# Optimization experiments

Measured on AMD Instinct MI355X. Metric: run time of the kernel, lower is better.

Reference implementation:

```python
import jax, jax.numpy as jnp
import numpy as np

EPS = 1e-5

def _layernorm(x, g, b):
    # normalize over last (channel) axis
    mu = jnp.mean(x, axis=-1, keepdims=True)
    var = jnp.var(x, axis=-1, keepdims=True)
    return (x - mu) * jax.lax.rsqrt(var + EPS) * g + b

def _dynamix(xt, wnd, bnd, wnn, bnn):
    # xt: [B, M, N, C]; mixes over the N axis (vectorized form of the per-slice loop)
    B, M, N, C = xt.shape
    d = wnd.shape[1]
    p = xt @ wnd + bnd                       # [B,M,N,d]
    p = p.reshape(B, M, N * d) @ wnn + bnn   # [B,M,N*N]
    p = jax.nn.softmax(p.reshape(B, M, N, N), axis=-1)
    return jnp.einsum('bmij,bmjc->bmic', p, xt)  # [B,M,N,C]

def setup_inputs() -> dict:
    key = jax.random.key(0)
    ks = jax.random.split(key, 10)
    B, C, H, W, d, E = 32, 128, 56, 56, 10, 4
    def n(k, shape, scale=0.02):
        return jax.random.normal(k, shape, jnp.float32) * scale
    return {
        'x': jax.random.normal(ks[0], (B, C, H, W), jnp.float32),
        'ln1_g': jnp.ones((C,), jnp.float32), 'ln1_b': jnp.zeros((C,), jnp.float32),
        'h_wnd': n(ks[1], (C, d)), 'h_bnd': jnp.zeros((d,), jnp.float32),
        'h_wnn': n(ks[2], (W * d, W * W)), 'h_bnn': jnp.zeros((W * W,), jnp.float32),
        'w_wnd': n(ks[3], (C, d)), 'w_bnd': jnp.zeros((d,), jnp.float32),
        'w_wnn': n(ks[4], (H * d, H * H)), 'w_bnn': jnp.zeros((H * H,), jnp.float32),
        'pc_w': n(ks[5], (C, C)), 'pc_b': jnp.zeros((C,), jnp.float32),
        'po_w': n(ks[6], (C, C)), 'po_b': jnp.zeros((C,), jnp.float32),
        'ln2_g': jnp.ones((C,), jnp.float32), 'ln2_b': jnp.zeros((C,), jnp.float32),
        'fc1_w': n(ks[7], (C, E * C)), 'fc1_b': jnp.zeros((E * C,), jnp.float32),
        'fc2_w': n(ks[8], (E * C, C)), 'fc2_b': jnp.zeros((C,), jnp.float32),
    }

def reference(x, ln1_g, ln1_b, h_wnd, h_bnd, h_wnn, h_bnn,
              w_wnd, w_bnd, w_wnn, w_bnn, pc_w, pc_b, po_w, po_b,
              ln2_g, ln2_b, fc1_w, fc1_b, fc2_w, fc2_b):
    # x: [B,C,H,W] -> work channels-last [B,H,W,C]
    xt = jnp.transpose(x, (0, 2, 3, 1))
    # ---- block p1: LN + DynaMixer ----
    u = _layernorm(xt, ln1_g, ln1_b)                 # [B,H,W,C]
    y_h = _dynamix(u, h_wnd, h_bnd, h_wnn, h_bnn)    # mix over W per row
    u_w = jnp.transpose(u, (0, 2, 1, 3))             # [B,W,H,C]
    y_w = _dynamix(u_w, w_wnd, w_bnd, w_wnn, w_bnn)  # mix over H per col
    y_w = jnp.transpose(y_w, (0, 2, 1, 3))           # back to [B,H,W,C]
    y_c = u @ pc_w + pc_b                            # 1x1 conv proj_c
    y = (y_h + y_w + y_c) @ po_w + po_b              # 1x1 conv proj_o
    xt = xt + y                                      # residual (drop_path=0)
    # ---- block p2: LN + MLP ----
    v = _layernorm(xt, ln2_g, ln2_b)
    h = jax.nn.gelu(v @ fc1_w + fc1_b, approximate=False)
    h = h @ fc2_w + fc2_b
    xt = xt + h
    return jnp.transpose(xt, (0, 3, 1, 2))           # [B,C,H,W]
```

## Files before the change

kernel.cpp:

```cpp
#include <hip/hip_runtime.h>
#include <math.h>

#define BB 32
#define CC 128
#define HH 56
#define WW 56
#define HWHW 3136
#define TOK 100352
#define BH 1792
#define NDP 576
#define NNP 3200

typedef __attribute__((ext_vector_type(8))) short bhalf8;
typedef __attribute__((ext_vector_type(4))) float f32x4;
typedef __attribute__((ext_vector_type(4))) unsigned int u32x4;

__device__ inline unsigned short f2bf(float f) {
  unsigned int x = __float_as_uint(f);
  unsigned int r = (x + 0x7FFFu + ((x >> 16) & 1u)) >> 16;
  return (unsigned short)r;
}
__device__ inline float bf2f(unsigned short u) {
  return __uint_as_float(((unsigned int)u) << 16);
}
__device__ inline unsigned int pack2(float a, float b) {
  return (unsigned int)f2bf(a) | ((unsigned int)f2bf(b) << 16);
}
__device__ inline f32x4 MFMA(bhalf8 a, bhalf8 b, f32x4 c) {
  return __builtin_amdgcn_mfma_f32_16x16x32_bf16(a, b, c, 0, 0, 0);
}
template <int CH>
__device__ inline bhalf8 ldsFrag(const unsigned short* base, int row, int chunk) {
  return *reinterpret_cast<const bhalf8*>(base + row * (CH * 8) + ((chunk ^ (row & 7)) * 8));
}
__device__ inline bhalf8 gFrag(const unsigned short* p) {
  return *reinterpret_cast<const bhalf8*>(p);
}
__device__ inline float gelu_f(float x) {
  float x3 = x * x * x;
  float z = 0.7978845608028654f * (x + 0.044715f * x3);
  float e = __expf(2.0f * z);
  float t = 1.0f - 2.0f / (e + 1.0f);
  return 0.5f * x * (1.0f + t);
}

__global__ __launch_bounds__(256) void wtrans_kernel(
    const float* __restrict__ hwnn, const float* __restrict__ wwnn,
    const float* __restrict__ pcw, const float* __restrict__ pow_,
    const float* __restrict__ fc1w, const float* __restrict__ fc2w,
    const float* __restrict__ hwnd, const float* __restrict__ wwnd,
    unsigned short* __restrict__ wnnTh, unsigned short* __restrict__ wnnTw,
    unsigned short* __restrict__ pcT, unsigned short* __restrict__ poT,
    unsigned short* __restrict__ fc1T, unsigned short* __restrict__ fc2T,
    unsigned short* __restrict__ wcatT, u32x4* __restrict__ pdzero) {
  __shared__ unsigned short t[64][65];
  int bid = blockIdx.x;
  int tid = threadIdx.x;
  if (bid >= 940) {
    int gt = (bid - 940) * 256 + tid, gs = 64 * 256;
    for (int i = gt; i < 258048; i += gs) { u32x4 z = {0, 0, 0, 0}; pdzero[i] = z; }
    for (int i = gt; i < 128 * 32; i += gs) {
      int k = i >> 5, n = i & 31;
      float v = n < 10 ? hwnd[k * 10 + n] : (n < 20 ? wwnd[k * 10 + (n - 10)] : 0.f);
      wcatT[n * 128 + k] = f2bf(v);
    }
    return;
  }
  const float* src; unsigned short* dst;
  int K, N, Kp, Np, bx, by;
  if (bid < 450)      { src = hwnn; dst = wnnTh; K = 560; N = 3136; Kp = 576; Np = 3200; int b = bid;       bx = b % 50; by = b / 50; }
  else if (bid < 900) { src = wwnn; dst = wnnTw; K = 560; N = 3136; Kp = 576; Np = 3200; int b = bid - 450; bx = b % 50; by = b / 50; }
  else if (bid < 904) { src = pcw;  dst = pcT;   K = 128; N = 128;  Kp = 128; Np = 128;  int b = bid - 900; bx = b % 2;  by = b / 2; }
  else if (bid < 908) { src = pow_; dst = poT;   K = 128; N = 128;  Kp = 128; Np = 128;  int b = bid - 904; bx = b % 2;  by = b / 2; }
  else if (bid < 924) { src = fc1w; dst = fc1T;  K = 128; N = 512;  Kp = 128; Np = 512;  int b = bid - 908; bx = b % 8;  by = b / 8; }
  else                { src = fc2w; dst = fc2T;  K = 512; N = 128;  Kp = 512; Np = 128;  int b = bid - 924; bx = b % 2;  by = b / 2; }
  int n0 = bx * 64, k0 = by * 64;
  for (int idx = tid; idx < 4096; idx += 256) {
    int kk = idx >> 6, nn = idx & 63;
    float v = (k0 + kk < K && n0 + nn < N) ? src[(size_t)(k0 + kk) * N + n0 + nn] : 0.f;
    t[nn][kk] = f2bf(v);
  }
  __syncthreads();
  for (int idx = tid; idx < 4096; idx += 256) {
    int nn = idx >> 6, kk = idx & 63;
    if (n0 + nn < Np && k0 + kk < Kp)
      dst[(size_t)(n0 + nn) * Kp + k0 + kk] = t[nn][kk];
  }
}

__global__ __launch_bounds__(256) void ln1_kernel(const float* __restrict__ x,
    const float* __restrict__ g, const float* __restrict__ bt,
    unsigned short* __restrict__ ubf, unsigned short* __restrict__ xcl) {
  int bh = blockIdx.x;
  int b = bh / HH, h = bh % HH;
  __shared__ float lds[WW][CC + 1];
  __shared__ float mu[WW], rs[WW];
  const float* xp = x + ((size_t)b * CC) * HWHW + (size_t)h * WW;
  for (int idx = threadIdx.x; idx < CC * WW; idx += 256) {
    int c = idx / WW, w = idx % WW;
    lds[w][c] = xp[(size_t)c * HWHW + w];
  }
  __syncthreads();
  if (threadIdx.x < WW) {
    int w = threadIdx.x;
    float s = 0.f, ss = 0.f;
    for (int c = 0; c < CC; ++c) { float v = lds[w][c]; s += v; ss += v * v; }
    float m = s * (1.0f / CC);
    float var = ss * (1.0f / CC) - m * m;
    mu[w] = m; rs[w] = rsqrtf(var + 1e-5f);
  }
  __syncthreads();
  unsigned short* up = ubf + (size_t)bh * (WW * CC);
  unsigned short* xc = xcl + (size_t)bh * (WW * CC);
  for (int idx = threadIdx.x; idx < WW * CC; idx += 256) {
    int w = idx >> 7, c = idx & 127;
    float v = lds[w][c];
    up[idx] = f2bf((v - mu[w]) * rs[w] * g[c] + bt[c]);
    xc[idx] = f2bf(v);
  }
}

__global__ __launch_bounds__(256) void pd_mfma(const unsigned short* __restrict__ ubf,
    const unsigned short* __restrict__ wcatT, const float* __restrict__ hbnd,
    const float* __restrict__ wbnd, unsigned short* __restrict__ pdh,
    unsigned short* __restrict__ pdw) {
  __shared__ __align__(16) unsigned short sU[64 * 128];
  __shared__ __align__(16) unsigned short sW[32 * 128];
  int tid = threadIdx.x;
  int tok0 = blockIdx.x * 64;
  #pragma unroll
  for (int i = 0; i < 4; ++i) {
    int s = i * 256 + tid; int r = s >> 4, c = s & 15;
    u32x4 v = *reinterpret_cast<const u32x4*>(ubf + (size_t)(tok0 + r) * 128 + c * 8);
    *reinterpret_cast<u32x4*>(sU + r * 128 + ((c ^ (r & 7)) * 8)) = v;
  }
  #pragma unroll
  for (int i = 0; i < 2; ++i) {
    int s = i * 256 + tid; int r = s >> 4, c = s & 15;
    u32x4 v = *reinterpret_cast<const u32x4*>(wcatT + (size_t)r * 128 + c * 8);
    *reinterpret_cast<u32x4*>(sW + r * 128 + ((c ^ (r & 7)) * 8)) = v;
  }
  __syncthreads();
  int wid = tid >> 6, lane = tid & 63, l16 = lane & 15, lk = lane >> 4;
  f32x4 acc[2] = {};
  #pragma unroll
  for (int kk = 0; kk < 4; ++kk) {
    bhalf8 a = ldsFrag<16>(sU, wid * 16 + l16, kk * 4 + lk);
    #pragma unroll
    for (int f = 0; f < 2; ++f) {
      bhalf8 b = ldsFrag<16>(sW, f * 16 + l16, kk * 4 + lk);
      acc[f] = MFMA(a, b, acc[f]);
    }
  }
  #pragma unroll
  for (int f = 0; f < 2; ++f) {
    int n = f * 16 + l16;
    #pragma unroll
    for (int r = 0; r < 4; ++r) {
      int tok = tok0 + wid * 16 + lk * 4 + r;
      float v = acc[f][r];
      if (n < 10) {
        pdh[((size_t)(tok / 56)) * NDP + (size_t)(tok % 56) * 10 + n] = f2bf(v + hbnd[n]);
      } else if (n < 20) {
        int b = tok / HWHW; int rem = tok % HWHW; int hh = rem / 56; int w = rem % 56;
        pdw[((size_t)(b * 56 + w)) * NDP + (size_t)hh * 10 + (n - 10)] = f2bf(v + wbnd[n - 10]);
      }
    }
  }
}

__global__ __launch_bounds__(256) void gemm_logits(
    const unsigned short* __restrict__ pdh, const unsigned short* __restrict__ pdw,
    const unsigned short* __restrict__ wnnTh, const unsigned short* __restrict__ wnnTw,
    const float* __restrict__ hbnn, const float* __restrict__ wbnn,
    unsigned short* __restrict__ ph, unsigned short* __restrict__ pwb) {
  __shared__ __align__(16) unsigned short sA[128 * 64];
  __shared__ __align__(16) unsigned short sB[128 * 64];
  int tid = threadIdx.x;
  int byr = blockIdx.y;
  const unsigned short* A; const unsigned short* BT; const float* bias; unsigned short* Cout;
  int row0;
  if (byr < 14) { A = pdh; BT = wnnTh; bias = hbnn; Cout = ph;  row0 = byr * 128; }
  else          { A = pdw; BT = wnnTw; bias = wbnn; Cout = pwb; row0 = (byr - 14) * 128; }
  int col0 = blockIdx.x * 128;
  int wid = tid >> 6, lane = tid & 63;
  int wm = wid >> 1, wn = wid & 1;
  int l16 = lane & 15, lk = lane >> 4;
  f32x4 acc[4][4] = {};
  for (int k0 = 0; k0 < NDP; k0 += 64) {
    #pragma unroll
    for (int i = 0; i < 4; ++i) {
      int s = i * 256 + tid; int r = s >> 3, c = s & 7;
      u32x4 v = *reinterpret_cast<const u32x4*>(A + (size_t)(row0 + r) * NDP + k0 + c * 8);
      *reinterpret_cast<u32x4*>(sA + r * 64 + ((c ^ (r & 7)) * 8)) = v;
    }
    #pragma unroll
    for (int i = 0; i < 4; ++i) {
      int s = i * 256 + tid; int r = s >> 3, c = s & 7;
      u32x4 v = *reinterpret_cast<const u32x4*>(BT + (size_t)(col0 + r) * NDP + k0 + c * 8);
      *reinterpret_cast<u32x4*>(sB + r * 64 + ((c ^ (r & 7)) * 8)) = v;
    }
    __syncthreads();
    bhalf8 af[4][2], bf[4][2];
    #pragma unroll
    for (int f = 0; f < 4; ++f)
      #pragma unroll
      for (int kk = 0; kk < 2; ++kk) {
        af[f][kk] = ldsFrag<8>(sA, wm * 64 + f * 16 + l16, kk * 4 + lk);
        bf[f][kk] = ldsFrag<8>(sB, wn * 64 + f * 16 + l16, kk * 4 + lk);
      }
    #pragma unroll
    for (int i = 0; i < 4; ++i)
      #pragma unroll
      for (int j = 0; j < 4; ++j) {
        acc[i][j] = MFMA(af[i][0], bf[j][0], acc[i][j]);
        acc[i][j] = MFMA(af[i][1], bf[j][1], acc[i][j]);
      }
    __syncthreads();
  }
  #pragma unroll
  for (int i = 0; i < 4; ++i) {
    int rbase = row0 + wm * 64 + i * 16 + lk * 4;
    #pragma unroll
    for (int j = 0; j < 4; ++j) {
      int col = col0 + wn * 64 + j * 16 + l16;
      if (col < HWHW) {
        float bv = bias[col];
        #pragma unroll
        for (int r = 0; r < 4; ++r)
          Cout[(size_t)(rbase + r) * NNP + col] = f2bf(acc[i][j][r] + bv);
      }
    }
  }
}

__global__ __launch_bounds__(256) void softmax56_kernel(unsigned short* __restrict__ ph,
                                                        unsigned short* __restrict__ pw) {
  int wave = (blockIdx.x * 256 + threadIdx.x) >> 6;
  int lane = threadIdx.x & 63;
  if (wave >= 2 * TOK) return;
  unsigned short* buf = wave < TOK ? ph : pw;
  int row = wave < TOK ? wave : wave - TOK;
  int bh = row / 56, i = row % 56;
  unsigned short* p = buf + (size_t)bh * NNP + (size_t)i * 56;
  float xv = lane < WW ? bf2f(p[lane]) : -INFINITY;
  float m = xv;
  for (int o = 32; o > 0; o >>= 1) m = fmaxf(m, __shfl_xor(m, o));
  float e = lane < WW ? __expf(xv - m) : 0.f;
  float s = e;
  for (int o = 32; o > 0; o >>= 1) s += __shfl_xor(s, o);
  if (lane < WW) p[lane] = f2bf(e / s);
}

__global__ __launch_bounds__(256) void mixh_pc(const unsigned short* __restrict__ ph,
    const unsigned short* __restrict__ ubf, const unsigned short* __restrict__ pcT,
    const float* __restrict__ pcb, unsigned short* __restrict__ accm) {
  int bh = blockIdx.x;
  int tok0 = bh * 56;
  __shared__ __align__(16) unsigned short sUt[128 * 64];
  int tid = threadIdx.x;
  for (int s = tid; s < 1024; s += 256) {
    int j = s >> 4, cc = s & 15;
    unsigned short e8[8] = {0, 0, 0, 0, 0, 0, 0, 0};
    if (j < 56)
      *reinterpret_cast<u32x4*>(e8) =
          *reinterpret_cast<const u32x4*>(ubf + (size_t)(tok0 + j) * 128 + cc * 8);
    #pragma unroll
    for (int e = 0; e < 8; ++e) {
      int cf = cc * 8 + e;
      sUt[cf * 64 + (((j >> 3) ^ (cf & 7)) * 8) + (j & 7)] = e8[e];
    }
  }
  __syncthreads();
  int lane = tid & 63, l16 = lane & 15, lk = lane >> 4, wn = tid >> 6;
  const unsigned short* prow = ph + (size_t)bh * NNP;
  f32x4 acc[4][2] = {};
  #pragma unroll
  for (int kk = 0; kk < 2; ++kk) {
    bhalf8 a[4], b[2];
    #pragma unroll
    for (int i = 0; i < 4; ++i)
      a[i] = gFrag(prow + (i * 16 + l16) * 56 + (kk * 4 + lk) * 8);
    #pragma unroll
    for (int j = 0; j < 2; ++j) b[j] = ldsFrag<8>(sUt, wn * 32 + j * 16 + l16, kk * 4 + lk);
    #pragma unroll
    for (int i = 0; i < 4; ++i)
      #pragma unroll
      for (int j = 0; j < 2; ++j) acc[i][j] = MFMA(a[i], b[j], acc[i][j]);
  }
  #pragma unroll
  for (int kk = 0; kk < 4; ++kk) {
    bhalf8 a[4], b[2];
    #pragma unroll
    for (int i = 0; i < 4; ++i)
      a[i] = gFrag(ubf + (size_t)(tok0 + i * 16 + l16) * 128 + (kk * 4 + lk) * 8);
    #pragma unroll
    for (int j = 0; j < 2; ++j)
      b[j] = gFrag(pcT + (size_t)(wn * 32 + j * 16 + l16) * 128 + (kk * 4 + lk) * 8);
    #pragma unroll
    for (int i = 0; i < 4; ++i)
      #pragma unroll
      for (int j = 0; j < 2; ++j) acc[i][j] = MFMA(a[i], b[j], acc[i][j]);
  }
  #pragma unroll
  for (int i = 0; i < 4; ++i) {
    int tok = i * 16 + lk * 4;
    #pragma unroll
    for (int j = 0; j < 2; ++j) {
      int c = wn * 32 + j * 16 + l16;
      float bv = pcb[c];
      #pragma unroll
      for (int r = 0; r < 4; ++r)
        if (tok + r < 56)
          accm[(size_t)(tok0 + tok + r) * 128 + c] = f2bf(acc[i][j][r] + bv);
    }
  }
}

__global__ __launch_bounds__(256) void mixw_fin(const unsigned short* __restrict__ pw,
    const unsigned short* __restrict__ ubf, const unsigned short* __restrict__ poT,
    const float* __restrict__ pob, const unsigned short* __restrict__ xcl,
    unsigned short* __restrict__ accXt,
    const float* __restrict__ ln2g, const float* __restrict__ ln2b,
    unsigned short* __restrict__ vbf) {
  int bw = blockIdx.x;
  int bq = bw / 56, w = bw % 56;
  __shared__ __align__(16) unsigned short sUt[128 * 64];
  __shared__ __align__(16) unsigned short sS[64 * 128];
  int tid = threadIdx.x;
  for (int s = tid; s < 1024; s += 256) {
    int j = s >> 4, cc = s & 15;
    unsigned short e8[8] = {0, 0, 0, 0, 0, 0, 0, 0};
    if (j < 56)
      *reinterpret_cast<u32x4*>(e8) =
          *reinterpret_cast<const u32x4*>(ubf + ((size_t)bq * HWHW + (size_t)j * 56 + w) * 128 + cc * 8);
    #pragma unroll
    for (int e = 0; e < 8; ++e) {
      int cf = cc * 8 + e;
      sUt[cf * 64 + (((j >> 3) ^ (cf & 7)) * 8) + (j & 7)] = e8[e];
    }
  }
  for (int s = tid; s < 1024; s += 256) {
    int r = s >> 4, c = s & 15;
    u32x4 v = {0, 0, 0, 0};
    if (r < 56) v = *reinterpret_cast<const u32x4*>(accXt + ((size_t)bq * HWHW + (size_t)r * 56 + w) * 128 + c * 8);
    *reinterpret_cast<u32x4*>(sS + r * 128 + ((c ^ (r & 7)) * 8)) = v;
  }
  __syncthreads();
  int lane = tid & 63, l16 = lane & 15, lk = lane >> 4, wn = tid >> 6;
  const unsigned short* prow = pw + (size_t)bw * NNP;
  f32x4 acc1[4][2] = {};
  #pragma unroll
  for (int kk = 0; kk < 2; ++kk) {
    bhalf8 a[4], b[2];
    #pragma unroll
    for (int i = 0; i < 4; ++i)
      a[i] = gFrag(prow + (i * 16 + l16) * 56 + (kk * 4 + lk) * 8);
    #pragma unroll
    for (int j = 0; j < 2; ++j) b[j] = ldsFrag<8>(sUt, wn * 32 + j * 16 + l16, kk * 4 + lk);
    #pragma unroll
    for (int i = 0; i < 4; ++i)
      #pragma unroll
      for (int j = 0; j < 2; ++j) acc1[i][j] = MFMA(a[i], b[j], acc1[i][j]);
  }
  __syncthreads();
  #pragma unroll
  for (int i = 0; i < 4; ++i) {
    #pragma unroll
    for (int j = 0; j < 2; ++j) {
      int col = wn * 32 + j * 16 + l16;
      #pragma unroll
      for (int r = 0; r < 4; ++r) {
        int row = i * 16 + lk * 4 + r;
        int ad = row * 128 + (((col >> 3) ^ (row & 7)) * 8) + (col & 7);
        sS[ad] = f2bf(bf2f(sS[ad]) + acc1[i][j][r]);
      }
    }
  }
  __syncthreads();
  f32x4 acc2[4][2] = {};
  #pragma unroll
  for (int kk = 0; kk < 4; ++kk) {
    bhalf8 a[4], b[2];
    #pragma unroll
    for (int i = 0; i < 4; ++i) a[i] = ldsFrag<16>(sS, i * 16 + l16, kk * 4 + lk);
    #pragma unroll
    for (int j = 0; j < 2; ++j)
      b[j] = gFrag(poT + (size_t)(wn * 32 + j * 16 + l16) * 128 + (kk * 4 + lk) * 8);
    #pragma unroll
    for (int i = 0; i < 4; ++i)
      #pragma unroll
      for (int j = 0; j < 2; ++j) acc2[i][j] = MFMA(a[i], b[j], acc2[i][j]);
  }
  __syncthreads();
  #pragma unroll
  for (int i = 0; i < 4; ++i) {
    #pragma unroll
    for (int j = 0; j < 2; ++j) {
      int c = wn * 32 + j * 16 + l16;
      float bv = pob[c];
      #pragma unroll
      for (int r = 0; r < 4; ++r) {
        int row = i * 16 + lk * 4 + r;
        if (row < 56) {
          size_t t = (size_t)bq * HWHW + (size_t)row * 56 + w;
          float z = acc2[i][j][r] + bv + bf2f(xcl[t * 128 + c]);
          unsigned short zb = f2bf(z);
          accXt[t * 128 + c] = zb;
          sS[row * 128 + (((c >> 3) ^ (row & 7)) * 8) + (c & 7)] = zb;
        }
      }
    }
  }
  __syncthreads();
  {
    int wid4 = tid >> 6;
    int c0 = 2 * lane;
    float g0 = ln2g[c0], g1 = ln2g[c0 + 1];
    float b0 = ln2b[c0], b1 = ln2b[c0 + 1];
    for (int row = wid4; row < 56; row += 4) {
      int ad = row * 128 + (((c0 >> 3) ^ (row & 7)) * 8) + (c0 & 7);
      unsigned int wrd = *reinterpret_cast<const unsigned int*>(sS + ad);
      float z0 = bf2f((unsigned short)(wrd & 0xFFFFu));
      float z1 = bf2f((unsigned short)(wrd >> 16));
      float s1 = z0 + z1, s2 = z0 * z0 + z1 * z1;
      for (int o = 32; o > 0; o >>= 1) { s1 += __shfl_xor(s1, o); s2 += __shfl_xor(s2, o); }
      float m = s1 * (1.0f / CC);
      float var = s2 * (1.0f / CC) - m * m;
      float rv = rsqrtf(var + 1e-5f);
      float n0 = (z0 - m) * rv * g0 + b0;
      float n1 = (z1 - m) * rv * g1 + b1;
      size_t t = (size_t)bq * HWHW + (size_t)row * 56 + w;
      *reinterpret_cast<unsigned int*>(vbf + t * 128 + c0) = pack2(n0, n1);
    }
  }
}

__global__ __launch_bounds__(256) void gemm_fc1(const unsigned short* __restrict__ vbf,
    const unsigned short* __restrict__ fc1T, const float* __restrict__ b1,
    unsigned short* __restrict__ hbuf) {
  __shared__ __align__(16) unsigned short sW[128 * 64];
  __shared__ __align__(16) unsigned short sV[128 * 64];
  __shared__ float b1s[128];
  int tid = threadIdx.x;
  int hidT = blockIdx.x * 128;
  int tok0 = blockIdx.y * 128;
  if (tid < 128) b1s[tid] = b1[hidT + tid];
  int wid = tid >> 6, lane = tid & 63;
  int wm = wid >> 1, wn = wid & 1;
  int l16 = lane & 15, lk = lane >> 4;
  f32x4 acc[4][4] = {};
  for (int k0 = 0; k0 < 128; k0 += 64) {
    #pragma unroll
    for (int i = 0; i < 4; ++i) {
      int s = i * 256 + tid; int r = s >> 3, c = s & 7;
      u32x4 v = *reinterpret_cast<const u32x4*>(fc1T + (size_t)(hidT + r) * 128 + k0 + c * 8);
      *reinterpret_cast<u32x4*>(sW + r * 64 + ((c ^ (r & 7)) * 8)) = v;
    }
    #pragma unroll
    for (int i = 0; i < 4; ++i) {
      int s = i * 256 + tid; int r = s >> 3, c = s & 7;
      u32x4 v = *reinterpret_cast<const u32x4*>(vbf + (size_t)(tok0 + r) * 128 + k0 + c * 8);
      *reinterpret_cast<u32x4*>(sV + r * 64 + ((c ^ (r & 7)) * 8)) = v;
    }
    __syncthreads();
    bhalf8 af[4][2], bf[4][2];
    #pragma unroll
    for (int f = 0; f < 4; ++f)
      #pragma unroll
      for (int kk = 0; kk < 2; ++kk) {
        af[f][kk] = ldsFrag<8>(sW, wm * 64 + f * 16 + l16, kk * 4 + lk);
        bf[f][kk] = ldsFrag<8>(sV, wn * 64 + f * 16 + l16, kk * 4 + lk);
      }
    #pragma unroll
    for (int i = 0; i < 4; ++i)
      #pragma unroll
      for (int j = 0; j < 4; ++j) {
        acc[i][j] = MFMA(af[i][0], bf[j][0], acc[i][j]);
        acc[i][j] = MFMA(af[i][1], bf[j][1], acc[i][j]);
      }
    __syncthreads();
  }
  #pragma unroll
  for (int i = 0; i < 4; ++i) {
    int hidL = wm * 64 + i * 16 + lk * 4;
    #pragma unroll
    for (int j = 0; j < 4; ++j) {
      int tokL = wn * 64 + j * 16 + l16;
      float v0 = gelu_f(acc[i][j][0] + b1s[hidL]);
      float v1 = gelu_f(acc[i][j][1] + b1s[hidL + 1]);
      float v2 = gelu_f(acc[i][j][2] + b1s[hidL + 2]);
      float v3 = gelu_f(acc[i][j][3] + b1s[hidL + 3]);
      unsigned long long pk = (unsigned long long)pack2(v0, v1)
                            | ((unsigned long long)pack2(v2, v3) << 32);
      *reinterpret_cast<unsigned long long*>(
          hbuf + (size_t)(tok0 + tokL) * 512 + hidT + hidL) = pk;
    }
  }
}

__global__ __launch_bounds__(256) void gemm_fc2(const unsigned short* __restrict__ hbuf,
    const unsigned short* __restrict__ fc2T, const float* __restrict__ b2,
    const unsigned short* __restrict__ xt2, float* __restrict__ out) {
  __shared__ __align__(16) unsigned short smem[2][128 * 64];
  __shared__ float b2s[128];
  unsigned short* sH = smem[0];
  unsigned short* sC = smem[1];
  unsigned short* xtile = &smem[0][0];
  int tid = threadIdx.x;
  int tok0 = blockIdx.x * 128;
  if (tid < 128) b2s[tid] = b2[tid];
  int wid = tid >> 6, lane = tid & 63;
  int wm = wid >> 1, wn = wid & 1;
  int l16 = lane & 15, lk = lane >> 4;
  f32x4 acc[4][4] = {};
  for (int k0 = 0; k0 < 512; k0 += 64) {
    #pragma unroll
    for (int i = 0; i < 4; ++i) {
      int s = i * 256 + tid; int r = s >> 3, c = s & 7;
      u32x4 v = *reinterpret_cast<const u32x4*>(hbuf + (size_t)(tok0 + r) * 512 + k0 + c * 8);
      *reinterpret_cast<u32x4*>(sH + r * 64 + ((c ^ (r & 7)) * 8)) = v;
    }
    #pragma unroll
    for (int i = 0; i < 4; ++i) {
      int s = i * 256 + tid; int r = s >> 3, c = s & 7;
      u32x4 v = *reinterpret_cast<const u32x4*>(fc2T + (size_t)r * 512 + k0 + c * 8);
      *reinterpret_cast<u32x4*>(sC + r * 64 + ((c ^ (r & 7)) * 8)) = v;
    }
    __syncthreads();
    bhalf8 af[4][2], bf[4][2];
    #pragma unroll
    for (int f = 0; f < 4; ++f)
      #pragma unroll
      for (int kk = 0; kk < 2; ++kk) {
        af[f][kk] = ldsFrag<8>(sH, wm * 64 + f * 16 + l16, kk * 4 + lk);
        bf[f][kk] = ldsFrag<8>(sC, wn * 64 + f * 16 + l16, kk * 4 + lk);
      }
    #pragma unroll
    for (int i = 0; i < 4; ++i)
      #pragma unroll
      for (int j = 0; j < 4; ++j) {
        acc[i][j] = MFMA(af[i][0], bf[j][0], acc[i][j]);
        acc[i][j] = MFMA(af[i][1], bf[j][1], acc[i][j]);
      }
    __syncthreads();
  }
  #pragma unroll
  for (int i = 0; i < 8; ++i) {
    int s = i * 256 + tid; int r = s >> 4, c = s & 15;
    u32x4 v = *reinterpret_cast<const u32x4*>(xt2 + (size_t)(tok0 + r) * 128 + c * 8);
    *reinterpret_cast<u32x4*>(xtile + r * 128 + c * 8) = v;
  }
  __syncthreads();
  #pragma unroll
  for (int i = 0; i < 4; ++i) {
    int tokL = wm * 64 + i * 16 + lk * 4;
    int tokG = tok0 + tokL;
    int bqv = tokG / HWHW;
    int pos = tokG - bqv * HWHW;
    #pragma unroll
    for (int j = 0; j < 4; ++j) {
      int cL = wn * 64 + j * 16 + l16;
      float bv = b2s[cL];
      f32x4 o;
      #pragma unroll
      for (int r = 0; r < 4; ++r)
        o[r] = acc[i][j][r] + bv + bf2f(xtile[(tokL + r) * 128 + cL]);
      *reinterpret_cast<f32x4*>(out + ((size_t)(bqv * CC + cL)) * HWHW + pos) = o;
    }
  }
}

extern "C" void kernel_launch(void* const* d_in, const int* in_sizes, int n_in,
                              void* d_out, int out_size, void* d_ws, size_t ws_size,
                              hipStream_t stream) {
  const float* x     = (const float*)d_in[0];
  const float* ln1_g = (const float*)d_in[1];
  const float* ln1_b = (const float*)d_in[2];
  const float* h_wnd = (const float*)d_in[3];
  const float* h_bnd = (const float*)d_in[4];
  const float* h_wnn = (const float*)d_in[5];
  const float* h_bnn = (const float*)d_in[6];
  const float* w_wnd = (const float*)d_in[7];
  const float* w_bnd = (const float*)d_in[8];
  const float* w_wnn = (const float*)d_in[9];
  const float* w_bnn = (const float*)d_in[10];
  const float* pc_w  = (const float*)d_in[11];
  const float* pc_b  = (const float*)d_in[12];
  const float* po_w  = (const float*)d_in[13];
  const float* po_b  = (const float*)d_in[14];
  const float* ln2_g = (const float*)d_in[15];
  const float* ln2_b = (const float*)d_in[16];
  const float* fc1_w = (const float*)d_in[17];
  const float* fc1_b = (const float*)d_in[18];
  const float* fc2_w = (const float*)d_in[19];
  const float* fc2_b = (const float*)d_in[20];
  float* out = (float*)d_out;
  char* ws = (char*)d_ws;

  unsigned short* ubf   = (unsigned short*)(ws + 0);
  unsigned short* xcl   = (unsigned short*)(ws + 25690112);
  unsigned short* accXt = (unsigned short*)(ws + 51380224);
  unsigned short* pdh   = (unsigned short*)(ws + 77070336);
  unsigned short* pdw   = (unsigned short*)(ws + 79134720);
  unsigned short* ph    = (unsigned short*)(ws + 81199104);
  unsigned short* pw    = (unsigned short*)(ws + 92667904);
  unsigned short* wnnTh = (unsigned short*)(ws + 104136704);
  unsigned short* wnnTw = (unsigned short*)(ws + 107823104);
  unsigned short* hbuf  = (unsigned short*)(ws + 77070336);
  unsigned short* pcT   = (unsigned short*)(ws + 179830784);
  unsigned short* poT   = (unsigned short*)(ws + 179863552);
  unsigned short* fc1T  = (unsigned short*)(ws + 179896320);
  unsigned short* fc2T  = (unsigned short*)(ws + 180027392);
  unsigned short* wcatT = (unsigned short*)(ws + 180158464);
  unsigned short* vbf   = ubf;

  wtrans_kernel<<<1004, 256, 0, stream>>>(h_wnn, w_wnn, pc_w, po_w, fc1_w, fc2_w,
      h_wnd, w_wnd, wnnTh, wnnTw, pcT, poT, fc1T, fc2T, wcatT, (u32x4*)pdh);
  ln1_kernel<<<BH, 256, 0, stream>>>(x, ln1_g, ln1_b, ubf, xcl);
  pd_mfma<<<TOK / 64, 256, 0, stream>>>(ubf, wcatT, h_bnd, w_bnd, pdh, pdw);
  gemm_logits<<<dim3(NNP / 128, 28), 256, 0, stream>>>(pdh, pdw, wnnTh, wnnTw,
      h_bnn, w_bnn, ph, pw);
  softmax56_kernel<<<(2 * TOK) / 4, 256, 0, stream>>>(ph, pw);
  mixh_pc<<<BH, 256, 0, stream>>>(ph, ubf, pcT, pc_b, accXt);
  mixw_fin<<<BB * WW, 256, 0, stream>>>(pw, ubf, poT, po_b, xcl, accXt,
      ln2_g, ln2_b, vbf);
  gemm_fc1<<<dim3(4, TOK / 128), 256, 0, stream>>>(vbf, fc1T, fc1_b, hbuf);
  gemm_fc2<<<TOK / 128, 256, 0, stream>>>(hbuf, fc2T, fc2_b, accXt, out);
}
```

Measured before the change: 287.2 us.

## Load MFMA fragments directly from global memory in fc1/fc2 GEMMs, skipping LDS staging

Both MLP GEMMs now load bf16 operand fragments straight from global memory into registers via gFrag instead of staging tiles through shared memory with syncthreads. fc1 also moves to a 1D grid with a block-index swizzle so neighbouring blocks in time share token tiles, and it reads bias straight from global. fc2 prefetches the residual tile into LDS before its main loop. The aim is to remove LDS round-trips and barriers. The trade-off is that operands are re-read by several waves through cache, and there is less explicit reuse.

```diff
diff --git a/kernel.cpp b/kernel.cpp
--- a/kernel.cpp
+++ b/kernel.cpp
@@ -439,58 +439,41 @@
 __global__ __launch_bounds__(256) void gemm_fc1(const unsigned short* __restrict__ vbf,
     const unsigned short* __restrict__ fc1T, const float* __restrict__ b1,
     unsigned short* __restrict__ hbuf) {
-  __shared__ __align__(16) unsigned short sW[128 * 64];
-  __shared__ __align__(16) unsigned short sV[128 * 64];
-  __shared__ float b1s[128];
-  int tid = threadIdx.x;
-  int hidT = blockIdx.x * 128;
-  int tok0 = blockIdx.y * 128;
-  if (tid < 128) b1s[tid] = b1[hidT + tid];
+  int n = blockIdx.x;
+  int sw = (n & 7) * 392 + (n >> 3);
+  int hidT = (sw & 3) * 128;
+  int tok0 = (sw >> 2) * 128;
+  int tid = threadIdx.x;
   int wid = tid >> 6, lane = tid & 63;
   int wm = wid >> 1, wn = wid & 1;
   int l16 = lane & 15, lk = lane >> 4;
   f32x4 acc[4][4] = {};
-  for (int k0 = 0; k0 < 128; k0 += 64) {
-    #pragma unroll
-    for (int i = 0; i < 4; ++i) {
-      int s = i * 256 + tid; int r = s >> 3, c = s & 7;
-      u32x4 v = *reinterpret_cast<const u32x4*>(fc1T + (size_t)(hidT + r) * 128 + k0 + c * 8);
-      *reinterpret_cast<u32x4*>(sW + r * 64 + ((c ^ (r & 7)) * 8)) = v;
-    }
-    #pragma unroll
-    for (int i = 0; i < 4; ++i) {
-      int s = i * 256 + tid; int r = s >> 3, c = s & 7;
-      u32x4 v = *reinterpret_cast<const u32x4*>(vbf + (size_t)(tok0 + r) * 128 + k0 + c * 8);
-      *reinterpret_cast<u32x4*>(sV + r * 64 + ((c ^ (r & 7)) * 8)) = v;
-    }
-    __syncthreads();
-    bhalf8 af[4][2], bf[4][2];
-    #pragma unroll
-    for (int f = 0; f < 4; ++f)
-      #pragma unroll
-      for (int kk = 0; kk < 2; ++kk) {
-        af[f][kk] = ldsFrag<8>(sW, wm * 64 + f * 16 + l16, kk * 4 + lk);
-        bf[f][kk] = ldsFrag<8>(sV, wn * 64 + f * 16 + l16, kk * 4 + lk);
-      }
-    #pragma unroll
-    for (int i = 0; i < 4; ++i)
-      #pragma unroll
-      for (int j = 0; j < 4; ++j) {
-        acc[i][j] = MFMA(af[i][0], bf[j][0], acc[i][j]);
-        acc[i][j] = MFMA(af[i][1], bf[j][1], acc[i][j]);
-      }
-    __syncthreads();
+  #pragma unroll
+  for (int kk = 0; kk < 4; ++kk) {
+    bhalf8 a[4], b[4];
+    #pragma unroll
+    for (int i = 0; i < 4; ++i)
+      a[i] = gFrag(fc1T + (size_t)(hidT + wm * 64 + i * 16 + l16) * 128 + (kk * 4 + lk) * 8);
+    #pragma unroll
+    for (int j = 0; j < 4; ++j)
+      b[j] = gFrag(vbf + (size_t)(tok0 + wn * 64 + j * 16 + l16) * 128 + (kk * 4 + lk) * 8);
+    #pragma unroll
+    for (int i = 0; i < 4; ++i)
+      #pragma unroll
+      for (int j = 0; j < 4; ++j)
+        acc[i][j] = MFMA(a[i], b[j], acc[i][j]);
   }
   #pragma unroll
   for (int i = 0; i < 4; ++i) {
     int hidL = wm * 64 + i * 16 + lk * 4;
+    f32x4 bv = *reinterpret_cast<const f32x4*>(b1 + hidT + hidL);
     #pragma unroll
     for (int j = 0; j < 4; ++j) {
       int tokL = wn * 64 + j * 16 + l16;
-      float v0 = gelu_f(acc[i][j][0] + b1s[hidL]);
-      float v1 = gelu_f(acc[i][j][1] + b1s[hidL + 1]);
-      float v2 = gelu_f(acc[i][j][2] + b1s[hidL + 2]);
-      float v3 = gelu_f(acc[i][j][3] + b1s[hidL + 3]);
+      float v0 = gelu_f(acc[i][j][0] + bv[0]);
+      float v1 = gelu_f(acc[i][j][1] + bv[1]);
+      float v2 = gelu_f(acc[i][j][2] + bv[2]);
+      float v3 = gelu_f(acc[i][j][3] + bv[3]);
       unsigned long long pk = (unsigned long long)pack2(v0, v1)
                             | ((unsigned long long)pack2(v2, v3) << 32);
       *reinterpret_cast<unsigned long long*>(
@@ -502,56 +485,37 @@
 __global__ __launch_bounds__(256) void gemm_fc2(const unsigned short* __restrict__ hbuf,
     const unsigned short* __restrict__ fc2T, const float* __restrict__ b2,
     const unsigned short* __restrict__ xt2, float* __restrict__ out) {
-  __shared__ __align__(16) unsigned short smem[2][128 * 64];
+  __shared__ __align__(16) unsigned short xtile[128 * 128];
   __shared__ float b2s[128];
-  unsigned short* sH = smem[0];
-  unsigned short* sC = smem[1];
-  unsigned short* xtile = &smem[0][0];
   int tid = threadIdx.x;
   int tok0 = blockIdx.x * 128;
   if (tid < 128) b2s[tid] = b2[tid];
+  #pragma unroll
+  for (int i = 0; i < 8; ++i) {
+    int s = i * 256 + tid; int r = s >> 4, c = s & 15;
+    u32x4 v = *reinterpret_cast<const u32x4*>(xt2 + (size_t)(tok0 + r) * 128 + c * 8);
+    *reinterpret_cast<u32x4*>(xtile + r * 128 + c * 8) = v;
+  }
+  __syncthreads();
   int wid = tid >> 6, lane = tid & 63;
   int wm = wid >> 1, wn = wid & 1;
   int l16 = lane & 15, lk = lane >> 4;
   f32x4 acc[4][4] = {};
-  for (int k0 = 0; k0 < 512; k0 += 64) {
-    #pragma unroll
-    for (int i = 0; i < 4; ++i) {
-      int s = i * 256 + tid; int r = s >> 3, c = s & 7;
-      u32x4 v = *reinterpret_cast<const u32x4*>(hbuf + (size_t)(tok0 + r) * 512 + k0 + c * 8);
-      *reinterpret_cast<u32x4*>(sH + r * 64 + ((c ^ (r & 7)) * 8)) = v;
-    }
-    #pragma unroll
-    for (int i = 0; i < 4; ++i) {
-      int s = i * 256 + tid; int r = s >> 3, c = s & 7;
-      u32x4 v = *reinterpret_cast<const u32x4*>(fc2T + (size_t)r * 512 + k0 + c * 8);
-      *reinterpret_cast<u32x4*>(sC + r * 64 + ((c ^ (r & 7)) * 8)) = v;
-    }
-    __syncthreads();
-    bhalf8 af[4][2], bf[4][2];
-    #pragma unroll
-    for (int f = 0; f < 4; ++f)
-      #pragma unroll
-      for (int kk = 0; kk < 2; ++kk) {
-        af[f][kk] = ldsFrag<8>(sH, wm * 64 + f * 16 + l16, kk * 4 + lk);
-        bf[f][kk] = ldsFrag<8>(sC, wn * 64 + f * 16 + l16, kk * 4 + lk);
-      }
-    #pragma unroll
-    for (int i = 0; i < 4; ++i)
-      #pragma unroll
-      for (int j = 0; j < 4; ++j) {
-        acc[i][j] = MFMA(af[i][0], bf[j][0], acc[i][j]);
-        acc[i][j] = MFMA(af[i][1], bf[j][1], acc[i][j]);
-      }
-    __syncthreads();
-  }
-  #pragma unroll
-  for (int i = 0; i < 8; ++i) {
-    int s = i * 256 + tid; int r = s >> 4, c = s & 15;
-    u32x4 v = *reinterpret_cast<const u32x4*>(xt2 + (size_t)(tok0 + r) * 128 + c * 8);
-    *reinterpret_cast<u32x4*>(xtile + r * 128 + c * 8) = v;
-  }
-  __syncthreads();
+  #pragma unroll 4
+  for (int ck = 0; ck < 16; ++ck) {
+    bhalf8 a[4], b[4];
+    #pragma unroll
+    for (int i = 0; i < 4; ++i)
+      a[i] = gFrag(hbuf + (size_t)(tok0 + wm * 64 + i * 16 + l16) * 512 + (ck * 4 + lk) * 8);
+    #pragma unroll
+    for (int j = 0; j < 4; ++j)
+      b[j] = gFrag(fc2T + (size_t)(wn * 64 + j * 16 + l16) * 512 + (ck * 4 + lk) * 8);
+    #pragma unroll
+    for (int i = 0; i < 4; ++i)
+      #pragma unroll
+      for (int j = 0; j < 4; ++j)
+        acc[i][j] = MFMA(a[i], b[j], acc[i][j]);
+  }
   #pragma unroll
   for (int i = 0; i < 4; ++i) {
     int tokL = wm * 64 + i * 16 + lk * 4;
@@ -625,6 +589,6 @@
   mixh_pc<<<BH, 256, 0, stream>>>(ph, ubf, pcT, pc_b, accXt);
   mixw_fin<<<BB * WW, 256, 0, stream>>>(pw, ubf, poT, po_b, xcl, accXt,
       ln2_g, ln2_b, vbf);
-  gemm_fc1<<<dim3(4, TOK / 128), 256, 0, stream>>>(vbf, fc1T, fc1_b, hbuf);
+  gemm_fc1<<<3136, 256, 0, stream>>>(vbf, fc1T, fc1_b, hbuf);
   gemm_fc2<<<TOK / 128, 256, 0, stream>>>(hbuf, fc2T, fc2_b, accXt, out);
 }
```

Result: slower. 335.7 us (+16.9%).

## Restructure fc1 GEMM to load token tile once and stream weights from global

Applied to the files above, without the earlier changes.

The fc1 GEMM now assigns each block a 128-token tile covering all 512 hidden outputs. Before, four blocks each reloaded the same activation tile. The full 128x128 activation tile is staged once in LDS, and the loop walks four hidden chunks. Weight fragments are read straight from global memory (likely L2-resident) with no LDS staging, which drops the per-k-step syncs. The cost is fewer blocks and weight loads now exposed to global-memory latency inside the MFMA loop.

```diff
diff --git a/kernel.cpp b/kernel.cpp
--- a/kernel.cpp
+++ b/kernel.cpp
@@ -439,62 +439,52 @@
 __global__ __launch_bounds__(256) void gemm_fc1(const unsigned short* __restrict__ vbf,
     const unsigned short* __restrict__ fc1T, const float* __restrict__ b1,
     unsigned short* __restrict__ hbuf) {
-  __shared__ __align__(16) unsigned short sW[128 * 64];
-  __shared__ __align__(16) unsigned short sV[128 * 64];
-  __shared__ float b1s[128];
+  __shared__ __align__(16) unsigned short sV[128 * 128];
   int tid = threadIdx.x;
-  int hidT = blockIdx.x * 128;
-  int tok0 = blockIdx.y * 128;
-  if (tid < 128) b1s[tid] = b1[hidT + tid];
+  int tok0 = blockIdx.x * 128;
+  #pragma unroll
+  for (int i = 0; i < 8; ++i) {
+    int s = i * 256 + tid; int r = s >> 4, c = s & 15;
+    u32x4 v = *reinterpret_cast<const u32x4*>(vbf + (size_t)(tok0 + r) * 128 + c * 8);
+    *reinterpret_cast<u32x4*>(sV + r * 128 + ((c ^ (r & 7)) * 8)) = v;
+  }
+  __syncthreads();
   int wid = tid >> 6, lane = tid & 63;
   int wm = wid >> 1, wn = wid & 1;
   int l16 = lane & 15, lk = lane >> 4;
-  f32x4 acc[4][4] = {};
-  for (int k0 = 0; k0 < 128; k0 += 64) {
+  for (int hc = 0; hc < 4; ++hc) {
+    f32x4 acc[4][4] = {};
+    #pragma unroll
+    for (int kk = 0; kk < 4; ++kk) {
+      bhalf8 a[4], b[4];
+      #pragma unroll
+      for (int i = 0; i < 4; ++i)
+        a[i] = gFrag(fc1T + (size_t)(hc * 128 + wm * 64 + i * 16 + l16) * 128 + (kk * 4 + lk) * 8);
+      #pragma unroll
+      for (int j = 0; j < 4; ++j)
+        b[j] = ldsFrag<16>(sV, wn * 64 + j * 16 + l16, kk * 4 + lk);
+      #pragma unroll
+      for (int i = 0; i < 4; ++i)
+        #pragma unroll
+        for (int j = 0; j < 4; ++j)
+          acc[i][j] = MFMA(a[i], b[j], acc[i][j]);
+    }
     #pragma unroll
     for (int i = 0; i < 4; ++i) {
-      int s = i * 256 + tid; int r = s >> 3, c = s & 7;
-      u32x4 v = *reinterpret_cast<const u32x4*>(fc1T + (size_t)(hidT + r) * 128 + k0 + c * 8);
-      *reinterpret_cast<u32x4*>(sW + r * 64 + ((c ^ (r & 7)) * 8)) = v;
-    }
-    #pragma unroll
-    for (int i = 0; i < 4; ++i) {
-      int s = i * 256 + tid; int r = s >> 3, c = s & 7;
-      u32x4 v = *reinterpret_cast<const u32x4*>(vbf + (size_t)(tok0 + r) * 128 + k0 + c * 8);
-      *reinterpret_cast<u32x4*>(sV + r * 64 + ((c ^ (r & 7)) * 8)) = v;
-    }
-    __syncthreads();
-    bhalf8 af[4][2], bf[4][2];
-    #pragma unroll
-    for (int f = 0; f < 4; ++f)
-      #pragma unroll
-      for (int kk = 0; kk < 2; ++kk) {
-        af[f][kk] = ldsFrag<8>(sW, wm * 64 + f * 16 + l16, kk * 4 + lk);
-        bf[f][kk] = ldsFrag<8>(sV, wn * 64 + f * 16 + l16, kk * 4 + lk);
-      }
-    #pragma unroll
-    for (int i = 0; i < 4; ++i)
+      int hidL = hc * 128 + wm * 64 + i * 16 + lk * 4;
+      f32x4 bv = *reinterpret_cast<const f32x4*>(b1 + hidL);
       #pragma unroll
       for (int j = 0; j < 4; ++j) {
-        acc[i][j] = MFMA(af[i][0], bf[j][0], acc[i][j]);
-        acc[i][j] = MFMA(af[i][1], bf[j][1], acc[i][j]);
-      }
-    __syncthreads();
-  }
-  #pragma unroll
-  for (int i = 0; i < 4; ++i) {
-    int hidL = wm * 64 + i * 16 + lk * 4;
-    #pragma unroll
-    for (int j = 0; j < 4; ++j) {
-      int tokL = wn * 64 + j * 16 + l16;
-      float v0 = gelu_f(acc[i][j][0] + b1s[hidL]);
-      float v1 = gelu_f(acc[i][j][1] + b1s[hidL + 1]);
-      float v2 = gelu_f(acc[i][j][2] + b1s[hidL + 2]);
-      float v3 = gelu_f(acc[i][j][3] + b1s[hidL + 3]);
-      unsigned long long pk = (unsigned long long)pack2(v0, v1)
-                            | ((unsigned long long)pack2(v2, v3) << 32);
-      *reinterpret_cast<unsigned long long*>(
-          hbuf + (size_t)(tok0 + tokL) * 512 + hidT + hidL) = pk;
+        int tokL = wn * 64 + j * 16 + l16;
+        float v0 = gelu_f(acc[i][j][0] + bv[0]);
+        float v1 = gelu_f(acc[i][j][1] + bv[1]);
+        float v2 = gelu_f(acc[i][j][2] + bv[2]);
+        float v3 = gelu_f(acc[i][j][3] + bv[3]);
+        unsigned long long pk = (unsigned long long)pack2(v0, v1)
+                              | ((unsigned long long)pack2(v2, v3) << 32);
+        *reinterpret_cast<unsigned long long*>(
+            hbuf + (size_t)(tok0 + tokL) * 512 + hidL) = pk;
+      }
     }
   }
 }
@@ -625,6 +615,6 @@
   mixh_pc<<<BH, 256, 0, stream>>>(ph, ubf, pcT, pc_b, accXt);
   mixw_fin<<<BB * WW, 256, 0, stream>>>(pw, ubf, poT, po_b, xcl, accXt,
       ln2_g, ln2_b, vbf);
-  gemm_fc1<<<dim3(4, TOK / 128), 256, 0, stream>>>(vbf, fc1T, fc1_b, hbuf);
+  gemm_fc1<<<TOK / 128, 256, 0, stream>>>(vbf, fc1T, fc1_b, hbuf);
   gemm_fc2<<<TOK / 128, 256, 0, stream>>>(hbuf, fc2T, fc2_b, accXt, out);
 }
```

Result: slower. 347.0 us (+20.8%).
